# Performance work log

Hardware: AMD Instinct MI355X
Metric: run time of the kernel (lower is better)

## Reference

```python
import jax, jax.numpy as jnp
import numpy as np


def _mlp(x, w1, b1, w2, b2):
    # x: [..., in]; torch Linear: y = x @ W.T + b; GELU is exact (erf) in torch default
    h = jax.nn.gelu(x @ w1.T + b1, approximate=False)
    return h @ w2.T + b2


def setup_inputs() -> dict:
    key = jax.random.key(0)
    ks = jax.random.split(key, 12)
    b, dim, e, h, w = 8, 64, 128, 256, 256
    nt, nb = 6, 8
    inp = {
        "x": jax.random.normal(ks[0], (b, dim, h, w), jnp.float32),
        "flux": jax.random.normal(ks[1], (b, e, h, w), jnp.float32),
        "prompt": jax.random.uniform(ks[2], (nt, nb, e), jnp.float32),
        "conv_w": jax.random.normal(ks[3], (e, e, 3, 3), jnp.float32) * 0.02,
        "b_fc1_w": jax.random.normal(ks[4], (nb, dim), jnp.float32) * 0.05,
        "b_fc1_b": jax.random.normal(ks[5], (nb,), jnp.float32) * 0.05,
        "b_fc2_w": jax.random.normal(ks[6], (nb, nb), jnp.float32) * 0.05,
        "b_fc2_b": jax.random.normal(ks[7], (nb,), jnp.float32) * 0.05,
        "t_fc1_w": jax.random.normal(ks[8], (nt, e), jnp.float32) * 0.05,
        "t_fc1_b": jax.random.normal(ks[9], (nt,), jnp.float32) * 0.05,
        "t_fc2_w": jax.random.normal(ks[10], (nt, nt), jnp.float32) * 0.05,
        "t_fc2_b": jax.random.normal(ks[11], (nt,), jnp.float32) * 0.05,
    }
    return inp


def reference(x, flux, prompt, conv_w, b_fc1_w, b_fc1_b, b_fc2_w, b_fc2_b,
              t_fc1_w, t_fc1_b, t_fc2_w, t_fc2_b):
    # x: [b, dim, h, w]; flux: [b, embed_dim, h, w]
    flux = jnp.where(jnp.isnan(flux), jnp.zeros_like(flux), flux)
    x_hw = jnp.transpose(x, (0, 2, 3, 1))       # [b,h,w,dim]
    flux_hw = jnp.transpose(flux, (0, 2, 3, 1))  # [b,h,w,e]

    # per-pixel routing weights (softmax over basis / task channels)
    x_basis = jax.nn.softmax(_mlp(x_hw, b_fc1_w, b_fc1_b, b_fc2_w, b_fc2_b), axis=-1)   # [b,h,w,nb]
    x_task = jax.nn.softmax(_mlp(flux_hw, t_fc1_w, t_fc1_b, t_fc2_w, t_fc2_b), axis=-1)  # [b,h,w,nt]

    # fused two-stage broadcast-multiply-reduce:
    # sum_t sum_k x_task[b,t,h,w] * x_basis[b,k,h,w] * prompt[t,k,e] -> [b,e,h,w]
    prompts = jnp.einsum('bhwt,bhwk,tke->behw', x_task, x_basis, prompt)

    # conv3x3, stride 1, padding 1, no bias (NCHW, OIHW)
    out = jax.lax.conv_general_dilated(
        prompts, conv_w, window_strides=(1, 1), padding=((1, 1), (1, 1)),
        dimension_numbers=('NCHW', 'OIHW', 'NCHW'))
    return out
```

## Files before the change

kernel.cpp:

```cpp
#include <hip/hip_runtime.h>
#include <hip/hip_bf16.h>
#include <math.h>

#define HW   65536
#define NPIX 524288
#define NB   8
#define NT   6
#define NC   48
#define DIM  64
#define EE   128
#define KSTEPS 14
#define KVALID 432
#define COLS 130

typedef short bf16x8 __attribute__((ext_vector_type(8)));
typedef float f32x4  __attribute__((ext_vector_type(4)));

__device__ __forceinline__ float gelu_exact(float v) {
    return 0.5f * v * (1.0f + erff(v * 0.70710678118654752f));
}

__device__ __forceinline__ unsigned pack_bf16(float v0, float v1) {
    __hip_bfloat16 h0 = __float2bfloat16(v0);
    __hip_bfloat16 h1 = __float2bfloat16(v1);
    return (unsigned)(*(unsigned short*)&h0) | ((unsigned)(*(unsigned short*)&h1) << 16);
}

__global__ __launch_bounds__(256) void fold_weights_kernel(
    const float* __restrict__ conv_w,
    const float* __restrict__ prompt,
    unsigned short* __restrict__ WfB)
{
    int f = blockIdx.x * 256 + threadIdx.x;
    int j    = f & 7;
    int lane = (f >> 3) & 63;
    int ob   = (f >> 9) & 7;
    int ks   = f >> 12;

    int o = ob * 16 + (lane & 15);
    int k = ks * 32 + ((lane >> 4) << 3) + j;

    float acc = 0.f;
    if (k < KVALID) {
        int tap = k / 48;
        int tk  = k - tap * 48;
        int dy = tap / 3;
        int dx = tap - dy * 3;
        const float* pw = conv_w + ((size_t)o * EE) * 9 + dy * 3 + dx;
        const float* pp = prompt + (size_t)tk * EE;
        #pragma unroll 4
        for (int e = 0; e < EE; ++e)
            acc += pw[(size_t)e * 9] * pp[e];
    }
    __hip_bfloat16 h = __float2bfloat16(acc);
    WfB[f] = *(unsigned short*)&h;
}

__global__ __launch_bounds__(256, 4) void routing_kernel(
    const float* __restrict__ x,
    const float* __restrict__ flux,
    const float* __restrict__ b1w, const float* __restrict__ b1b,
    const float* __restrict__ b2w, const float* __restrict__ b2b,
    const float* __restrict__ t1w, const float* __restrict__ t1b,
    const float* __restrict__ t2w, const float* __restrict__ t2b,
    uint4* __restrict__ c2)
{
    __shared__ float s_b1w[DIM * 8];
    __shared__ float s_t1w[EE * 8];
    __shared__ float s_b2w[64];
    __shared__ float s_t2w[36];
    __shared__ float s_b1b[8], s_b2b[8], s_t1b[8], s_t2b[8];
    __shared__ float s_tsk[256][25];

    int tid = threadIdx.x;
    for (int i = tid; i < DIM * 8; i += 256) {
        int ci = i >> 3, j = i & 7;
        s_b1w[i] = b1w[j * DIM + ci];
    }
    for (int i = tid; i < EE * 8; i += 256) {
        int ci = i >> 3, j = i & 7;
        s_t1w[i] = (j < NT) ? t1w[j * EE + ci] : 0.f;
    }
    if (tid < 64) s_b2w[tid] = b2w[tid];
    if (tid < 36) s_t2w[tid] = t2w[tid];
    if (tid < 8) {
        s_b1b[tid] = b1b[tid];
        s_b2b[tid] = b2b[tid];
        s_t1b[tid] = (tid < NT) ? t1b[tid] : 0.f;
        s_t2b[tid] = (tid < NT) ? t2b[tid] : 0.f;
    }
    __syncthreads();

    int gq   = blockIdx.x * 256 + tid;
    int pix0 = gq << 2;
    int b    = pix0 >> 16;
    int yx   = pix0 & (HW - 1);

    const float* fp = flux + (size_t)b * EE * HW + yx;
    const float* xp = x + (size_t)b * DIM * HW + yx;

    float t[4][6];
    #pragma unroll
    for (int p = 0; p < 4; ++p)
        #pragma unroll
        for (int j = 0; j < NT; ++j) t[p][j] = s_t1b[j];

    #pragma unroll 1
    for (int cb = 0; cb < EE; cb += 8) {
        float4 v[8];
        #pragma unroll
        for (int u = 0; u < 8; ++u)
            v[u] = *(const float4*)(fp + (size_t)(cb + u) * HW);
        #pragma unroll
        for (int u = 0; u < 8; ++u) {
            float pv[4] = {v[u].x, v[u].y, v[u].z, v[u].w};
            const float* wp = &s_t1w[(cb + u) * 8];
            float4 wA = *(const float4*)wp;
            float2 wB = *(const float2*)(wp + 4);
            #pragma unroll
            for (int p = 0; p < 4; ++p) {
                float f = pv[p];
                f = (f == f) ? f : 0.f;
                t[p][0] += f * wA.x;
                t[p][1] += f * wA.y;
                t[p][2] += f * wA.z;
                t[p][3] += f * wA.w;
                t[p][4] += f * wB.x;
                t[p][5] += f * wB.y;
            }
        }
    }

    #pragma unroll
    for (int p = 0; p < 4; ++p)
        #pragma unroll
        for (int j = 0; j < NT; ++j)
            s_tsk[tid][p * 6 + j] = t[p][j];

    float a[4][8];
    #pragma unroll
    for (int p = 0; p < 4; ++p)
        #pragma unroll
        for (int j = 0; j < 8; ++j) a[p][j] = s_b1b[j];

    #pragma unroll 1
    for (int cb = 0; cb < DIM; cb += 8) {
        float4 v[8];
        #pragma unroll
        for (int u = 0; u < 8; ++u)
            v[u] = *(const float4*)(xp + (size_t)(cb + u) * HW);
        #pragma unroll
        for (int u = 0; u < 8; ++u) {
            float pv[4] = {v[u].x, v[u].y, v[u].z, v[u].w};
            const float* wp = &s_b1w[(cb + u) * 8];
            float4 wa = *(const float4*)wp;
            float4 wb = *(const float4*)(wp + 4);
            #pragma unroll
            for (int p = 0; p < 4; ++p) {
                float f = pv[p];
                a[p][0] += f * wa.x;
                a[p][1] += f * wa.y;
                a[p][2] += f * wa.z;
                a[p][3] += f * wa.w;
                a[p][4] += f * wb.x;
                a[p][5] += f * wb.y;
                a[p][6] += f * wb.z;
                a[p][7] += f * wb.w;
            }
        }
    }

    #pragma unroll
    for (int p = 0; p < 4; ++p) {
        float task[6];
        {
            float gt[6];
            #pragma unroll
            for (int j = 0; j < NT; ++j) gt[j] = gelu_exact(s_tsk[tid][p * 6 + j]);
            float tv[6];
            #pragma unroll
            for (int i = 0; i < NT; ++i) {
                float s = s_t2b[i];
                #pragma unroll
                for (int j = 0; j < NT; ++j) s += gt[j] * s_t2w[i * 6 + j];
                tv[i] = s;
            }
            float m = tv[0];
            #pragma unroll
            for (int i = 1; i < NT; ++i) m = fmaxf(m, tv[i]);
            float s = 0.f;
            #pragma unroll
            for (int i = 0; i < NT; ++i) { tv[i] = expf(tv[i] - m); s += tv[i]; }
            float inv = 1.f / s;
            #pragma unroll
            for (int i = 0; i < NT; ++i) task[i] = tv[i] * inv;
        }

        float basis[8];
        {
            float g[8];
            #pragma unroll
            for (int j = 0; j < 8; ++j) g[j] = gelu_exact(a[p][j]);
            float bv[8];
            #pragma unroll
            for (int i = 0; i < 8; ++i) {
                float s = s_b2b[i];
                #pragma unroll
                for (int j = 0; j < 8; ++j) s += g[j] * s_b2w[i * 8 + j];
                bv[i] = s;
            }
            float m = bv[0];
            #pragma unroll
            for (int i = 1; i < 8; ++i) m = fmaxf(m, bv[i]);
            float s = 0.f;
            #pragma unroll
            for (int i = 0; i < 8; ++i) { bv[i] = expf(bv[i] - m); s += bv[i]; }
            float inv = 1.f / s;
            #pragma unroll
            for (int i = 0; i < 8; ++i) basis[i] = bv[i] * inv;
        }

        #pragma unroll
        for (int j = 0; j < 6; ++j) {
            uint4 q;
            q.x = pack_bf16(task[j] * basis[0], task[j] * basis[1]);
            q.y = pack_bf16(task[j] * basis[2], task[j] * basis[3]);
            q.z = pack_bf16(task[j] * basis[4], task[j] * basis[5]);
            q.w = pack_bf16(task[j] * basis[6], task[j] * basis[7]);
            c2[(size_t)j * NPIX + pix0 + p] = q;
        }
    }
}

__global__ __launch_bounds__(256, 3) void conv_kernel(
    const uint4* __restrict__ c2,
    const unsigned short* __restrict__ WfB,
    float* __restrict__ out)
{
    __shared__ uint4 tile4[3120];

    int bid = blockIdx.x;
    int s = bid & 1;
    int y = (bid >> 1) & 255;
    int b = bid >> 9;
    int x0 = s << 7;
    int tid = threadIdx.x;

    #pragma unroll 4
    for (int i = tid; i < 3120; i += 256)
        tile4[i] = make_uint4(0u, 0u, 0u, 0u);
    __syncthreads();

    for (int idx = tid; idx < 2340; idx += 256) {
        int dyc = idx / 130;
        int col = idx - dyc * 130;
        int dy  = dyc / 6;
        int ch  = dyc - dy * 6;
        int gy = y + dy - 1;
        int gx = x0 - 1 + col;
        if ((unsigned)gy < 256u && (unsigned)gx < 256u) {
            uint4 v = c2[(size_t)ch * NPIX + (((size_t)b << 16) + (gy << 8) + gx)];
            int lb = ((dy * COLS + col) << 7) + (ch << 4);
            lb ^= (col & 7) << 4;
            tile4[lb >> 4] = v;
        }
    }
    __syncthreads();

    int lane = tid & 63;
    int wv = tid >> 6;
    int wm = wv & 1;
    int wn = wv >> 1;
    int o0 = wm << 6;
    int nbase = wn << 2;
    int lrow = lane & 15;
    int lk   = lane >> 4;

    f32x4 acc[4][4];
    #pragma unroll
    for (int mi = 0; mi < 4; ++mi)
        #pragma unroll
        for (int ni = 0; ni < 4; ++ni)
            acc[mi][ni] = (f32x4){0.f, 0.f, 0.f, 0.f};

    const char* tbase = (const char*)tile4;

    #pragma unroll
    for (int ks = 0; ks < KSTEPS; ++ks) {
        bf16x8 a[4];
        #pragma unroll
        for (int mi = 0; mi < 4; ++mi)
            a[mi] = *(const bf16x8*)(WfB + ((size_t)((ks * 8) + wm * 4 + mi) * 64 + lane) * 8);

        int k0 = ks * 32 + (lk << 3);
        int tap = k0 / 48;
        if (tap > 8) tap = 8;
        int ch = k0 - tap * 48;
        int dy = tap / 3;
        int dx = tap - dy * 3;

        #pragma unroll
        for (int ni = 0; ni < 4; ++ni) {
            int col = ((nbase + ni) << 4) + lrow + dx;
            int lb = ((dy * COLS + col) << 7) + (ch << 1);
            lb ^= (col & 7) << 4;
            bf16x8 bfr = *(const bf16x8*)(tbase + lb);
            #pragma unroll
            for (int mi = 0; mi < 4; ++mi)
                acc[mi][ni] = __builtin_amdgcn_mfma_f32_16x16x32_bf16(a[mi], bfr, acc[mi][ni], 0, 0, 0);
        }
    }

    int orow = lk << 2;
    #pragma unroll
    for (int mi = 0; mi < 4; ++mi) {
        #pragma unroll
        for (int ni = 0; ni < 4; ++ni) {
            int o = o0 + mi * 16 + orow;
            int xx = x0 + ((nbase + ni) << 4) + lrow;
            float* op = out + (((size_t)(b * 128 + o)) << 16) + (y << 8) + xx;
            #pragma unroll
            for (int r = 0; r < 4; ++r)
                op[(size_t)r << 16] = acc[mi][ni][r];
        }
    }
}

extern "C" void kernel_launch(void* const* d_in, const int* in_sizes, int n_in,
                              void* d_out, int out_size, void* d_ws, size_t ws_size,
                              hipStream_t stream) {
    const float* x      = (const float*)d_in[0];
    const float* flux   = (const float*)d_in[1];
    const float* prompt = (const float*)d_in[2];
    const float* conv_w = (const float*)d_in[3];
    const float* b1w    = (const float*)d_in[4];
    const float* b1b    = (const float*)d_in[5];
    const float* b2w    = (const float*)d_in[6];
    const float* b2b    = (const float*)d_in[7];
    const float* t1w    = (const float*)d_in[8];
    const float* t1b    = (const float*)d_in[9];
    const float* t2w    = (const float*)d_in[10];
    const float* t2b    = (const float*)d_in[11];
    float* out = (float*)d_out;

    char* ws = (char*)d_ws;
    uint4* c2 = (uint4*)ws;
    unsigned short* WfB = (unsigned short*)(ws + (size_t)6 * NPIX * 16);

    fold_weights_kernel<<<224, 256, 0, stream>>>(conv_w, prompt, WfB);
    routing_kernel<<<512, 256, 0, stream>>>(x, flux, b1w, b1b, b2w, b2b,
                                            t1w, t1b, t2w, t2b, c2);
    conv_kernel<<<4096, 256, 0, stream>>>(c2, WfB, out);
}
```

Baseline: 262.7 us.

## Split routing kernel into flux-MLP and basis-epilogue kernels with 128-thread blocks

The fused routing kernel is split into two kernels. The first computes the flux first-layer projections and writes the raw pre-activations to workspace. The second computes the basis MLP, reads those pre-activations back, and finishes the GELU/softmax epilogue into c2. Block size drops to 128 and the large shared s_tsk staging array is removed, which should ease register and LDS pressure and raise occupancy. The cost is an extra kernel launch and an extra global write and read of 6×NPIX floats, about 25 MB.

```diff
diff --git a/kernel.cpp b/kernel.cpp
--- a/kernel.cpp
+++ b/kernel.cpp
@@ -56,48 +56,27 @@
     WfB[f] = *(unsigned short*)&h;
 }
 
-__global__ __launch_bounds__(256, 4) void routing_kernel(
-    const float* __restrict__ x,
+__global__ __launch_bounds__(128) void flux_mlp_kernel(
     const float* __restrict__ flux,
-    const float* __restrict__ b1w, const float* __restrict__ b1b,
-    const float* __restrict__ b2w, const float* __restrict__ b2b,
     const float* __restrict__ t1w, const float* __restrict__ t1b,
-    const float* __restrict__ t2w, const float* __restrict__ t2b,
-    uint4* __restrict__ c2)
+    float* __restrict__ traw)
 {
-    __shared__ float s_b1w[DIM * 8];
     __shared__ float s_t1w[EE * 8];
-    __shared__ float s_b2w[64];
-    __shared__ float s_t2w[36];
-    __shared__ float s_b1b[8], s_b2b[8], s_t1b[8], s_t2b[8];
-    __shared__ float s_tsk[256][25];
+    __shared__ float s_t1b[8];
 
     int tid = threadIdx.x;
-    for (int i = tid; i < DIM * 8; i += 256) {
-        int ci = i >> 3, j = i & 7;
-        s_b1w[i] = b1w[j * DIM + ci];
-    }
-    for (int i = tid; i < EE * 8; i += 256) {
+    for (int i = tid; i < EE * 8; i += 128) {
         int ci = i >> 3, j = i & 7;
         s_t1w[i] = (j < NT) ? t1w[j * EE + ci] : 0.f;
     }
-    if (tid < 64) s_b2w[tid] = b2w[tid];
-    if (tid < 36) s_t2w[tid] = t2w[tid];
-    if (tid < 8) {
-        s_b1b[tid] = b1b[tid];
-        s_b2b[tid] = b2b[tid];
-        s_t1b[tid] = (tid < NT) ? t1b[tid] : 0.f;
-        s_t2b[tid] = (tid < NT) ? t2b[tid] : 0.f;
-    }
+    if (tid < 8) s_t1b[tid] = (tid < NT) ? t1b[tid] : 0.f;
     __syncthreads();
 
-    int gq   = blockIdx.x * 256 + tid;
+    int gq   = blockIdx.x * 128 + tid;
     int pix0 = gq << 2;
     int b    = pix0 >> 16;
     int yx   = pix0 & (HW - 1);
-
     const float* fp = flux + (size_t)b * EE * HW + yx;
-    const float* xp = x + (size_t)b * DIM * HW + yx;
 
     float t[4][6];
     #pragma unroll
@@ -113,10 +92,10 @@
             v[u] = *(const float4*)(fp + (size_t)(cb + u) * HW);
         #pragma unroll
         for (int u = 0; u < 8; ++u) {
-            float pv[4] = {v[u].x, v[u].y, v[u].z, v[u].w};
             const float* wp = &s_t1w[(cb + u) * 8];
             float4 wA = *(const float4*)wp;
             float2 wB = *(const float2*)(wp + 4);
+            float pv[4] = {v[u].x, v[u].y, v[u].z, v[u].w};
             #pragma unroll
             for (int p = 0; p < 4; ++p) {
                 float f = pv[p];
@@ -132,10 +111,44 @@
     }
 
     #pragma unroll
-    for (int p = 0; p < 4; ++p)
-        #pragma unroll
-        for (int j = 0; j < NT; ++j)
-            s_tsk[tid][p * 6 + j] = t[p][j];
+    for (int j = 0; j < NT; ++j) {
+        float4 q = make_float4(t[0][j], t[1][j], t[2][j], t[3][j]);
+        *(float4*)&traw[(size_t)j * NPIX + pix0] = q;
+    }
+}
+
+__global__ __launch_bounds__(128) void basis_epilogue_kernel(
+    const float* __restrict__ x,
+    const float* __restrict__ traw,
+    const float* __restrict__ b1w, const float* __restrict__ b1b,
+    const float* __restrict__ b2w, const float* __restrict__ b2b,
+    const float* __restrict__ t2w, const float* __restrict__ t2b,
+    uint4* __restrict__ c2)
+{
+    __shared__ float s_b1w[DIM * 8];
+    __shared__ float s_b2w[64];
+    __shared__ float s_t2w[36];
+    __shared__ float s_b1b[8], s_b2b[8], s_t2b[8];
+
+    int tid = threadIdx.x;
+    for (int i = tid; i < DIM * 8; i += 128) {
+        int ci = i >> 3, j = i & 7;
+        s_b1w[i] = b1w[j * DIM + ci];
+    }
+    if (tid < 64) s_b2w[tid] = b2w[tid];
+    if (tid < 36) s_t2w[tid] = t2w[tid];
+    if (tid < 8) {
+        s_b1b[tid] = b1b[tid];
+        s_b2b[tid] = b2b[tid];
+        s_t2b[tid] = (tid < NT) ? t2b[tid] : 0.f;
+    }
+    __syncthreads();
+
+    int gq   = blockIdx.x * 128 + tid;
+    int pix0 = gq << 2;
+    int b    = pix0 >> 16;
+    int yx   = pix0 & (HW - 1);
+    const float* xp = x + (size_t)b * DIM * HW + yx;
 
     float a[4][8];
     #pragma unroll
@@ -151,10 +164,10 @@
             v[u] = *(const float4*)(xp + (size_t)(cb + u) * HW);
         #pragma unroll
         for (int u = 0; u < 8; ++u) {
-            float pv[4] = {v[u].x, v[u].y, v[u].z, v[u].w};
             const float* wp = &s_b1w[(cb + u) * 8];
             float4 wa = *(const float4*)wp;
             float4 wb = *(const float4*)(wp + 4);
+            float pv[4] = {v[u].x, v[u].y, v[u].z, v[u].w};
             #pragma unroll
             for (int p = 0; p < 4; ++p) {
                 float f = pv[p];
@@ -170,13 +183,21 @@
         }
     }
 
+    float4 tj[6];
+    #pragma unroll
+    for (int j = 0; j < NT; ++j)
+        tj[j] = *(const float4*)&traw[(size_t)j * NPIX + pix0];
+
     #pragma unroll
     for (int p = 0; p < 4; ++p) {
         float task[6];
         {
             float gt[6];
             #pragma unroll
-            for (int j = 0; j < NT; ++j) gt[j] = gelu_exact(s_tsk[tid][p * 6 + j]);
+            for (int j = 0; j < NT; ++j) {
+                float tv = (p == 0) ? tj[j].x : (p == 1) ? tj[j].y : (p == 2) ? tj[j].z : tj[j].w;
+                gt[j] = gelu_exact(tv);
+            }
             float tv[6];
             #pragma unroll
             for (int i = 0; i < NT; ++i) {
@@ -346,9 +367,11 @@
     char* ws = (char*)d_ws;
     uint4* c2 = (uint4*)ws;
     unsigned short* WfB = (unsigned short*)(ws + (size_t)6 * NPIX * 16);
+    float* traw = (float*)(ws + (size_t)6 * NPIX * 16 + 131072);
 
     fold_weights_kernel<<<224, 256, 0, stream>>>(conv_w, prompt, WfB);
-    routing_kernel<<<512, 256, 0, stream>>>(x, flux, b1w, b1b, b2w, b2b,
-                                            t1w, t1b, t2w, t2b, c2);
+    flux_mlp_kernel<<<1024, 128, 0, stream>>>(flux, t1w, t1b, traw);
+    basis_epilogue_kernel<<<1024, 128, 0, stream>>>(x, traw, b1w, b1b, b2w, b2b,
+                                                    t2w, t2b, c2);
     conv_kernel<<<4096, 256, 0, stream>>>(c2, WfB, out);
 }
```

Measured after the change: 273.6 us. 1.04x slower.
